# Kernel tuning notes

Hardware: AMD Instinct MI355X
Metric: run time of the kernel (lower is better)

## Reference

```python
import jax, jax.numpy as jnp
import numpy as np

TOPK = 2  # config.expert_topk


def setup_inputs() -> dict:
    key = jax.random.key(0)
    k1, k2, k3, k4 = jax.random.split(key, 4)
    B, T, D, H, E = 2, 2048, 768, 3072, 8
    x = jax.random.normal(k1, (B, T, D), jnp.float32)
    gate_w = jax.random.normal(k2, (E, D), jnp.float32) * 0.02   # nn.Linear(D, E).weight
    w_fc = jax.random.normal(k3, (E, H, D), jnp.float32) * 0.02  # per-expert c_fc.weight [out,in]
    w_proj = jax.random.normal(k4, (E, D, H), jnp.float32) * 0.02  # per-expert c_proj.weight
    return {"x": x, "gate_w": gate_w, "w_fc": w_fc, "w_proj": w_proj}


def reference(x, gate_w, w_fc, w_proj):
    # x: [B,T,D]; gate_w: [E,D]; w_fc: [E,H,D]; w_proj: [E,D,H]
    B, T, D = x.shape
    E = gate_w.shape[0]
    N = B * T
    xf = x.reshape(N, D)

    gate_logits = xf @ gate_w.T                       # [N,E]
    gate_probs = jax.nn.softmax(gate_logits, axis=-1)
    rw, idx = jax.lax.top_k(gate_probs, TOPK)          # [N,k]
    rw = rw / jnp.sum(rw, axis=-1, keepdims=True)

    # combine[n,e] = sum_k rw[n,k] * (idx[n,k]==e); zero for unselected experts,
    # so the dense per-expert MLP below computes the same math as torch dispatch.
    oh = jax.nn.one_hot(idx, E, dtype=xf.dtype)        # [N,k,E]
    combine = jnp.einsum('nk,nke->ne', rw, oh)         # [N,E]

    h = jnp.einsum('nd,ehd->neh', xf, w_fc)            # [N,E,H]
    h = jnp.square(jax.nn.relu(h))                     # relu(x)^2
    y = jnp.einsum('neh,edh->ned', h, w_proj)          # [N,E,D]
    out = jnp.einsum('ned,ne->nd', y, combine).reshape(B, T, D)

    # expert_freq = bincount(expert_indices)/N, detached in the loss
    counts = jnp.sum(oh, axis=(0, 1))                  # [E]
    expert_freq = counts / N
    balance_loss = jnp.sum(gate_probs.mean(axis=0) * jax.lax.stop_gradient(expert_freq)) * E
    return out, balance_loss
```

## Files before the change

kernel.cpp:

```cpp
#include <hip/hip_runtime.h>
#include <hip/hip_bf16.h>

typedef __bf16 bf16_t;
typedef bf16_t bf16x8 __attribute__((ext_vector_type(8)));
typedef bf16_t bf16x4 __attribute__((ext_vector_type(4)));
typedef float f32x4 __attribute__((ext_vector_type(4)));

#define N_TOK 4096
#define DIM   768
#define HID   3072
#define NEXP  8
#define PADROWS 9216
#define MMAX  32
#define MT2   64

#define OFF_COUNTS 0
#define OFF_PSUM   32
#define OFF_OFFPAD 64
#define OFF_CURSOR 128
#define OFF_TOKE   256
#define OFF_TOKW   (OFF_TOKE + 4*8192)
#define OFF_PERMT  (OFF_TOKW + 4*8192)
#define OFF_PERMW  (OFF_PERMT + 4*PADROWS)
#define OFF_XP     (((OFF_PERMW + 4*PADROWS) + 511) & ~511ull)
#define OFF_WFC    (OFF_XP + 2ull*PADROWS*DIM)
#define OFF_WPJ    (OFF_WFC + 2ull*NEXP*HID*DIM)
#define OFF_H      (OFF_WPJ + 2ull*NEXP*DIM*HID)
#define WS_NEEDED  (OFF_H + 2ull*PADROWS*HID)

#define CONV_BLOCKS 9216
#define GATE_BLOCKS (N_TOK / 4)

__device__ __forceinline__ void async_copy16(const bf16_t* g, bf16_t* l) {
    __builtin_amdgcn_global_load_lds(
        (const __attribute__((address_space(1))) void*)g,
        (__attribute__((address_space(3))) void*)l, 16, 0, 0);
}

__global__ __launch_bounds__(256) void prep_kernel(
    const float* __restrict__ w_fc, const float* __restrict__ w_proj,
    bf16_t* __restrict__ wfc_b, bf16_t* __restrict__ wpj_b,
    const float* __restrict__ x, const float* __restrict__ gw,
    int* __restrict__ cs_part, float* __restrict__ ps_part,
    int* __restrict__ tok_e, float* __restrict__ tok_w)
{
    __shared__ float ps[8];
    __shared__ int cs[8];

    if (blockIdx.x >= GATE_BLOCKS) {
        const int cid = blockIdx.x - GATE_BLOCKS;
        const int half_blocks = CONV_BLOCKS / 2;
        const bool second = cid >= half_blocks;
        const float* src = second ? w_proj : w_fc;
        bf16_t* dst = second ? wpj_b : wfc_b;
        const long long bid = second ? (cid - half_blocks) : cid;
        const long long base = bid * 256 + threadIdx.x;
        const long long stride = (long long)half_blocks * 256;
#pragma unroll
        for (int it = 0; it < 4; it++) {
            const long long i4 = base + (long long)it * stride;
            float4 v = *((const float4*)src + i4);
            bf16x4 o;
            o[0] = (bf16_t)v.x; o[1] = (bf16_t)v.y;
            o[2] = (bf16_t)v.z; o[3] = (bf16_t)v.w;
            *(bf16x4*)(dst + i4 * 4) = o;
        }
        return;
    }

    if (threadIdx.x < 8) { ps[threadIdx.x] = 0.f; cs[threadIdx.x] = 0; }
    __syncthreads();

    const int bid = blockIdx.x;
    const int wv = threadIdx.x >> 6, lane = threadIdx.x & 63;
    const int n = bid * 4 + wv;

    float acc[8];
#pragma unroll
    for (int e = 0; e < 8; e++) acc[e] = 0.f;
    const float* xr = x + (size_t)n * DIM;
#pragma unroll
    for (int c = 0; c < 12; c++) {
        const float xv = xr[c * 64 + lane];
#pragma unroll
        for (int e = 0; e < 8; e++) acc[e] += xv * gw[e * DIM + c * 64 + lane];
    }
#pragma unroll
    for (int e = 0; e < 8; e++)
        for (int off = 32; off > 0; off >>= 1) acc[e] += __shfl_xor(acc[e], off, 64);

    float mx = acc[0];
#pragma unroll
    for (int e = 1; e < 8; e++) mx = fmaxf(mx, acc[e]);
    float p[8], s = 0.f;
#pragma unroll
    for (int e = 0; e < 8; e++) { p[e] = expf(acc[e] - mx); s += p[e]; }

    int e1 = 0;
#pragma unroll
    for (int e = 1; e < 8; e++) if (p[e] > p[e1]) e1 = e;
    int e2 = (e1 == 0) ? 1 : 0;
#pragma unroll
    for (int e = 0; e < 8; e++) if (e != e1 && p[e] > p[e2]) e2 = e;
    const float denom = p[e1] + p[e2];

    if (lane == 0) {
        tok_e[2 * n] = e1; tok_e[2 * n + 1] = e2;
        tok_w[2 * n] = p[e1] / denom; tok_w[2 * n + 1] = p[e2] / denom;
        const float inv = 1.f / s;
#pragma unroll
        for (int e = 0; e < 8; e++) atomicAdd(&ps[e], p[e] * inv);
        atomicAdd(&cs[e1], 1); atomicAdd(&cs[e2], 1);
    }
    __syncthreads();
    if (threadIdx.x < 8) {
        ps_part[bid * 8 + threadIdx.x] = ps[threadIdx.x];
        cs_part[bid * 8 + threadIdx.x] = cs[threadIdx.x];
    }
}

__global__ __launch_bounds__(256) void finalize_scatter(
    const int* cs_part, const float* ps_part,
    const int* __restrict__ tok_e, const float* __restrict__ tok_w,
    int* __restrict__ counts, int* __restrict__ off_pad,
    int* perm_tok, int* inv_pos, float* __restrict__ out_loss)
{
    __shared__ float rps[256];
    __shared__ int rcs[256];
    __shared__ int s_cur[8];
    const int t = threadIdx.x;
    const int e = t & 7, chunk = t >> 3;
    float psum = 0.f; int csum = 0;
#pragma unroll
    for (int i = 0; i < 32; i++) {
        const int b = chunk * 32 + i;
        psum += ps_part[b * 8 + e];
        csum += cs_part[b * 8 + e];
    }
    rps[t] = psum; rcs[t] = csum;
    __syncthreads();
    for (int s = 128; s >= 8; s >>= 1) {
        if (t < s) { rps[t] += rps[t + s]; rcs[t] += rcs[t + s]; }
        __syncthreads();
    }
    if (t == 0) {
        int off = 0; float loss = 0.f;
        for (int k = 0; k < 8; k++) {
            counts[k] = rcs[k];
            off_pad[k] = off; s_cur[k] = off;
            off += ((rcs[k] + 127) & ~127);
            loss += rps[k] * (float)rcs[k];
        }
        off_pad[8] = off;
        *out_loss = loss * 8.f / ((float)N_TOK * (float)N_TOK);
    }
    __syncthreads();
    for (int r = 0; r < N_TOK / 256; r++) {
        const int n = r * 256 + t;
#pragma unroll
        for (int k = 0; k < 2; k++) {
            const int ee = tok_e[2 * n + k];
            const int pos = atomicAdd(&s_cur[ee], 1);
            perm_tok[pos] = n;
            inv_pos[2 * n + k] = pos;
        }
    }
}

__global__ __launch_bounds__(256) void gather_x_kernel(
    const float* __restrict__ x, const int* __restrict__ off_pad,
    const int* __restrict__ counts, const int* __restrict__ perm_tok,
    bf16_t* __restrict__ xp)
{
    __shared__ int so[9], scnt[8];
    if (threadIdx.x < 9) so[threadIdx.x] = off_pad[threadIdx.x];
    if (threadIdx.x < 8) scnt[threadIdx.x] = counts[threadIdx.x];
    __syncthreads();
    const int gid = blockIdx.x * 256 + threadIdx.x;
    const int p = gid / 192;
    const int c = (gid - p * 192) * 4;
    int e = 0;
#pragma unroll
    for (int k = 1; k < 8; k++) if (p >= so[k]) e = k;
    const bool valid = (p < so[8]) && (p - so[e] < scnt[e]);
    float4 v = make_float4(0.f, 0.f, 0.f, 0.f);
    if (valid) {
        const int tok = perm_tok[p];
        v = *(const float4*)(x + (size_t)tok * DIM + c);
    }
    bf16x4 o; o[0] = (bf16_t)v.x; o[1] = (bf16_t)v.y; o[2] = (bf16_t)v.z; o[3] = (bf16_t)v.w;
    *(bf16x4*)(xp + (size_t)p * DIM + c) = o;
}

__global__ __launch_bounds__(256, 3) void gemm1_kernel(
    const bf16_t* __restrict__ xp, const bf16_t* __restrict__ wfc,
    const int* __restrict__ off_pad, bf16_t* __restrict__ h)
{
    const int id = blockIdx.x;
    const int e = id & 7;
    const int slot = id >> 3;
    const int n_t = slot / MMAX, m_t = slot % MMAX;

    const int seg0 = off_pad[e];
    const int cnt_pad = off_pad[e + 1] - seg0;
    const int m0 = m_t * 128;
    if (m0 >= cnt_pad) return;
    const int n0 = n_t * 128;

    __shared__ bf16_t As[128 * 64];
    __shared__ bf16_t Bs[128 * 64];

    const int t = threadIdx.x;
    const int srow = t >> 3, sc = t & 7;
    const int gsc = sc ^ (srow & 7);
    const bf16_t* abase = xp + (size_t)(seg0 + m0 + srow) * DIM + gsc * 8;
    const bf16_t* bbase = wfc + ((size_t)e * HID + n0 + srow) * DIM + gsc * 8;

    const int wv = t >> 6, lane = t & 63;
    const int lrow = lane & 15, quad = lane >> 4;
    const int wm = (wv & 1) * 64, wn = (wv >> 1) * 64;
    const int sw = lrow & 7;

    f32x4 acc[4][4] = {};

    for (int k0 = 0; k0 < DIM; k0 += 64) {
        __syncthreads();
#pragma unroll
        for (int ii = 0; ii < 4; ii++) {
            async_copy16(abase + (size_t)ii * 32 * DIM + k0, &As[(ii * 256 + t) * 8]);
            async_copy16(bbase + (size_t)ii * 32 * DIM + k0, &Bs[(ii * 256 + t) * 8]);
        }
        __syncthreads();
#pragma unroll
        for (int kh = 0; kh < 2; kh++) {
            const int ch = ((kh * 4 + quad) ^ sw) * 8;
            bf16x8 af[4], bfv[4];
#pragma unroll
            for (int i = 0; i < 4; i++)
                af[i] = *(bf16x8*)&As[(wm + i * 16 + lrow) * 64 + ch];
#pragma unroll
            for (int j = 0; j < 4; j++)
                bfv[j] = *(bf16x8*)&Bs[(wn + j * 16 + lrow) * 64 + ch];
#pragma unroll
            for (int i = 0; i < 4; i++)
#pragma unroll
                for (int j = 0; j < 4; j++)
                    acc[i][j] = __builtin_amdgcn_mfma_f32_16x16x32_bf16(af[i], bfv[j], acc[i][j], 0, 0, 0);
        }
    }

#pragma unroll
    for (int i = 0; i < 4; i++) {
#pragma unroll
        for (int g = 0; g < 4; g++) {
            const int m = m0 + wm + i * 16 + quad * 4 + g;
            bf16_t* hrow = h + (size_t)(seg0 + m) * HID + n0 + wn + lrow;
#pragma unroll
            for (int j = 0; j < 4; j++) {
                float v = fmaxf(acc[i][j][g], 0.f);
                hrow[j * 16] = (bf16_t)(v * v);
            }
        }
    }
}

__global__ __launch_bounds__(256, 3) void gemm2_kernel(
    const bf16_t* __restrict__ h, const bf16_t* __restrict__ wpj,
    const int* __restrict__ off_pad, const int* __restrict__ counts,
    bf16_t* __restrict__ y)
{
    const int id = blockIdx.x;
    const int e = id & 7;
    const int slot = id >> 3;
    const int m_t = slot / 6, n_t = slot % 6;

    const int seg0 = off_pad[e];
    const int cnt = counts[e];
    const int m0 = m_t * 64;
    if (m0 >= cnt) return;
    const int n0 = n_t * 128;

    __shared__ bf16_t As[64 * 128];
    __shared__ bf16_t Bs[128 * 128];

    const int t = threadIdx.x;
    const int srow = t >> 4, sc = t & 15;
    const int gsc = sc ^ (srow & 7);
    const bf16_t* abase = h + (size_t)(seg0 + m0 + srow) * HID + gsc * 8;
    const bf16_t* bbase = wpj + ((size_t)e * DIM + n0 + srow) * HID + gsc * 8;

    const int wv = t >> 6, lane = t & 63;
    const int lrow = lane & 15, quad = lane >> 4;
    const int wm = (wv & 1) * 32, wn = (wv >> 1) * 64;
    const int sw = lrow & 7;

    f32x4 acc[2][4] = {};

    for (int k0 = 0; k0 < HID; k0 += 128) {
        __syncthreads();
#pragma unroll
        for (int ii = 0; ii < 4; ii++)
            async_copy16(abase + (size_t)ii * 16 * HID + k0, &As[(ii * 256 + t) * 8]);
#pragma unroll
        for (int ii = 0; ii < 8; ii++)
            async_copy16(bbase + (size_t)ii * 16 * HID + k0, &Bs[(ii * 256 + t) * 8]);
        __syncthreads();
#pragma unroll
        for (int kh = 0; kh < 4; kh++) {
            const int ch = ((kh * 4 + quad) ^ sw) * 8;
            bf16x8 af[2], bfv[4];
#pragma unroll
            for (int i = 0; i < 2; i++)
                af[i] = *(bf16x8*)&As[(wm + i * 16 + lrow) * 128 + ch];
#pragma unroll
            for (int j = 0; j < 4; j++)
                bfv[j] = *(bf16x8*)&Bs[(wn + j * 16 + lrow) * 128 + ch];
#pragma unroll
            for (int i = 0; i < 2; i++)
#pragma unroll
                for (int j = 0; j < 4; j++)
                    acc[i][j] = __builtin_amdgcn_mfma_f32_16x16x32_bf16(af[i], bfv[j], acc[i][j], 0, 0, 0);
        }
    }

#pragma unroll
    for (int i = 0; i < 2; i++) {
#pragma unroll
        for (int g = 0; g < 4; g++) {
            const int m = m0 + wm + i * 16 + quad * 4 + g;
            if (m < cnt) {
                bf16_t* yrow = y + (size_t)(seg0 + m) * DIM + n0 + wn + lrow;
#pragma unroll
                for (int j = 0; j < 4; j++)
                    yrow[j * 16] = (bf16_t)acc[i][j][g];
            }
        }
    }
}

__global__ __launch_bounds__(192) void combine_kernel(
    const bf16_t* __restrict__ y, const int* __restrict__ inv_pos,
    const float* __restrict__ tok_w, float* __restrict__ out)
{
    const int n = blockIdx.x;
    const int d = threadIdx.x * 4;
    const int p1 = inv_pos[2 * n], p2 = inv_pos[2 * n + 1];
    const float w1 = tok_w[2 * n], w2 = tok_w[2 * n + 1];
    bf16x4 a = *(const bf16x4*)(y + (size_t)p1 * DIM + d);
    bf16x4 b = *(const bf16x4*)(y + (size_t)p2 * DIM + d);
    float4 o;
    o.x = w1 * (float)a[0] + w2 * (float)b[0];
    o.y = w1 * (float)a[1] + w2 * (float)b[1];
    o.z = w1 * (float)a[2] + w2 * (float)b[2];
    o.w = w1 * (float)a[3] + w2 * (float)b[3];
    *(float4*)(out + (size_t)n * DIM + d) = o;
}

extern "C" void kernel_launch(void* const* d_in, const int* in_sizes, int n_in,
                              void* d_out, int out_size, void* d_ws, size_t ws_size,
                              hipStream_t stream) {
    const float* x      = (const float*)d_in[0];
    const float* gate_w = (const float*)d_in[1];
    const float* w_fc   = (const float*)d_in[2];
    const float* w_proj = (const float*)d_in[3];
    float* out = (float*)d_out;

    if (ws_size < WS_NEEDED) return;

    char* w = (char*)d_ws;
    int*    counts    = (int*)(w + OFF_COUNTS);
    int*    off_pad   = (int*)(w + OFF_OFFPAD);
    int*    tok_e     = (int*)(w + OFF_TOKE);
    float*  tok_w     = (float*)(w + OFF_TOKW);
    int*    perm_tok  = (int*)(w + OFF_PERMT);
    int*    inv_pos   = (int*)(w + OFF_PERMW);
    bf16_t* xp        = (bf16_t*)(w + OFF_XP);
    bf16_t* wfc_b     = (bf16_t*)(w + OFF_WFC);
    bf16_t* wpj_b     = (bf16_t*)(w + OFF_WPJ);
    bf16_t* hbuf      = (bf16_t*)(w + OFF_H);

    int*   cs_part = perm_tok;
    float* ps_part = (float*)inv_pos;
    bf16_t* y = xp;

    hipMemsetAsync(d_out, 0, (size_t)out_size * sizeof(float), stream);

    prep_kernel<<<GATE_BLOCKS + CONV_BLOCKS, 256, 0, stream>>>(
        w_fc, w_proj, wfc_b, wpj_b, x, gate_w, cs_part, ps_part, tok_e, tok_w);
    finalize_scatter<<<1, 256, 0, stream>>>(cs_part, ps_part, tok_e, tok_w,
                                            counts, off_pad, perm_tok, inv_pos,
                                            out + (size_t)out_size - 1);
    gather_x_kernel<<<PADROWS * DIM / 4 / 256, 256, 0, stream>>>(x, off_pad, counts, perm_tok, xp);

    gemm1_kernel<<<8 * 24 * MMAX, 256, 0, stream>>>(xp, wfc_b, off_pad, hbuf);
    gemm2_kernel<<<8 * MT2 * 6, 256, 0, stream>>>(hbuf, wpj_b, off_pad, counts, y);
    combine_kernel<<<N_TOK, 192, 0, stream>>>(y, inv_pos, tok_w, out);
}
```

Measured before the change: 337.6 us.

## Overlap w_proj conversion with gemm1 and split gemm2 LDS tiles into halves

Converting w_proj to bf16 moves out of the prep kernel and into extra trailing blocks of the gemm1 launch. The aim is to overlap that bandwidth-bound conversion with the expert GEMM and to shorten the critical prep phase. Separately, gemm2's 128-wide K tile in LDS is split into two 64-wide sub-tiles so the 8-chunk XOR swizzle covers each row fully, which reduces LDS bank conflicts. The extra conversion blocks compete with gemm1 blocks for CUs and may delay the GEMM tail.

```diff
diff --git a/kernel.cpp b/kernel.cpp
--- a/kernel.cpp
+++ b/kernel.cpp
@@ -28,8 +28,9 @@
 #define OFF_H      (OFF_WPJ + 2ull*NEXP*DIM*HID)
 #define WS_NEEDED  (OFF_H + 2ull*PADROWS*HID)
 
-#define CONV_BLOCKS 9216
 #define GATE_BLOCKS (N_TOK / 4)
+#define CONVH_BLOCKS 4608
+#define GEMM1_BLOCKS (8 * 24 * MMAX)
 
 __device__ __forceinline__ void async_copy16(const bf16_t* g, bf16_t* l) {
     __builtin_amdgcn_global_load_lds(
@@ -37,9 +38,24 @@
         (__attribute__((address_space(3))) void*)l, 16, 0, 0);
 }
 
+__device__ __forceinline__ void convert_chunk(const float* __restrict__ src,
+                                              bf16_t* __restrict__ dst,
+                                              int cid, int t) {
+    const long long base = (long long)cid * 256 + t;
+    const long long stride = (long long)CONVH_BLOCKS * 256;
+#pragma unroll
+    for (int it = 0; it < 4; it++) {
+        const long long i4 = base + (long long)it * stride;
+        float4 v = *((const float4*)src + i4);
+        bf16x4 o;
+        o[0] = (bf16_t)v.x; o[1] = (bf16_t)v.y;
+        o[2] = (bf16_t)v.z; o[3] = (bf16_t)v.w;
+        *(bf16x4*)(dst + i4 * 4) = o;
+    }
+}
+
 __global__ __launch_bounds__(256) void prep_kernel(
-    const float* __restrict__ w_fc, const float* __restrict__ w_proj,
-    bf16_t* __restrict__ wfc_b, bf16_t* __restrict__ wpj_b,
+    const float* __restrict__ w_fc, bf16_t* __restrict__ wfc_b,
     const float* __restrict__ x, const float* __restrict__ gw,
     int* __restrict__ cs_part, float* __restrict__ ps_part,
     int* __restrict__ tok_e, float* __restrict__ tok_w)
@@ -48,23 +64,7 @@
     __shared__ int cs[8];
 
     if (blockIdx.x >= GATE_BLOCKS) {
-        const int cid = blockIdx.x - GATE_BLOCKS;
-        const int half_blocks = CONV_BLOCKS / 2;
-        const bool second = cid >= half_blocks;
-        const float* src = second ? w_proj : w_fc;
-        bf16_t* dst = second ? wpj_b : wfc_b;
-        const long long bid = second ? (cid - half_blocks) : cid;
-        const long long base = bid * 256 + threadIdx.x;
-        const long long stride = (long long)half_blocks * 256;
-#pragma unroll
-        for (int it = 0; it < 4; it++) {
-            const long long i4 = base + (long long)it * stride;
-            float4 v = *((const float4*)src + i4);
-            bf16x4 o;
-            o[0] = (bf16_t)v.x; o[1] = (bf16_t)v.y;
-            o[2] = (bf16_t)v.z; o[3] = (bf16_t)v.w;
-            *(bf16x4*)(dst + i4 * 4) = o;
-        }
+        convert_chunk(w_fc, wfc_b, blockIdx.x - GATE_BLOCKS, threadIdx.x);
         return;
     }
 
@@ -194,9 +194,14 @@
 
 __global__ __launch_bounds__(256, 3) void gemm1_kernel(
     const bf16_t* __restrict__ xp, const bf16_t* __restrict__ wfc,
-    const int* __restrict__ off_pad, bf16_t* __restrict__ h)
+    const int* __restrict__ off_pad, bf16_t* __restrict__ h,
+    const float* __restrict__ w_proj, bf16_t* __restrict__ wpj_b)
 {
     const int id = blockIdx.x;
+    if (id >= GEMM1_BLOCKS) {
+        convert_chunk(w_proj, wpj_b, id - GEMM1_BLOCKS, threadIdx.x);
+        return;
+    }
     const int e = id & 7;
     const int slot = id >> 3;
     const int n_t = slot / MMAX, m_t = slot % MMAX;
@@ -280,11 +285,11 @@
     if (m0 >= cnt) return;
     const int n0 = n_t * 128;
 
-    __shared__ bf16_t As[64 * 128];
-    __shared__ bf16_t Bs[128 * 128];
+    __shared__ bf16_t As[2][64 * 64];
+    __shared__ bf16_t Bs[2][128 * 64];
 
     const int t = threadIdx.x;
-    const int srow = t >> 4, sc = t & 15;
+    const int srow = t >> 3, sc = t & 7;
     const int gsc = sc ^ (srow & 7);
     const bf16_t* abase = h + (size_t)(seg0 + m0 + srow) * HID + gsc * 8;
     const bf16_t* bbase = wpj + ((size_t)e * DIM + n0 + srow) * HID + gsc * 8;
@@ -299,22 +304,28 @@
     for (int k0 = 0; k0 < HID; k0 += 128) {
         __syncthreads();
 #pragma unroll
-        for (int ii = 0; ii < 4; ii++)
-            async_copy16(abase + (size_t)ii * 16 * HID + k0, &As[(ii * 256 + t) * 8]);
-#pragma unroll
-        for (int ii = 0; ii < 8; ii++)
-            async_copy16(bbase + (size_t)ii * 16 * HID + k0, &Bs[(ii * 256 + t) * 8]);
+        for (int p = 0; p < 2; p++) {
+#pragma unroll
+            for (int ii = 0; ii < 2; ii++)
+                async_copy16(abase + (size_t)ii * 32 * HID + k0 + p * 64,
+                             &As[p][(ii * 256 + t) * 8]);
+#pragma unroll
+            for (int ii = 0; ii < 4; ii++)
+                async_copy16(bbase + (size_t)ii * 32 * HID + k0 + p * 64,
+                             &Bs[p][(ii * 256 + t) * 8]);
+        }
         __syncthreads();
 #pragma unroll
         for (int kh = 0; kh < 4; kh++) {
-            const int ch = ((kh * 4 + quad) ^ sw) * 8;
+            const int p = kh >> 1, khh = kh & 1;
+            const int ch = ((khh * 4 + quad) ^ sw) * 8;
             bf16x8 af[2], bfv[4];
 #pragma unroll
             for (int i = 0; i < 2; i++)
-                af[i] = *(bf16x8*)&As[(wm + i * 16 + lrow) * 128 + ch];
+                af[i] = *(bf16x8*)&As[p][(wm + i * 16 + lrow) * 64 + ch];
 #pragma unroll
             for (int j = 0; j < 4; j++)
-                bfv[j] = *(bf16x8*)&Bs[(wn + j * 16 + lrow) * 128 + ch];
+                bfv[j] = *(bf16x8*)&Bs[p][(wn + j * 16 + lrow) * 64 + ch];
 #pragma unroll
             for (int i = 0; i < 2; i++)
 #pragma unroll
@@ -385,14 +396,15 @@
 
     hipMemsetAsync(d_out, 0, (size_t)out_size * sizeof(float), stream);
 
-    prep_kernel<<<GATE_BLOCKS + CONV_BLOCKS, 256, 0, stream>>>(
-        w_fc, w_proj, wfc_b, wpj_b, x, gate_w, cs_part, ps_part, tok_e, tok_w);
+    prep_kernel<<<GATE_BLOCKS + CONVH_BLOCKS, 256, 0, stream>>>(
+        w_fc, wfc_b, x, gate_w, cs_part, ps_part, tok_e, tok_w);
     finalize_scatter<<<1, 256, 0, stream>>>(cs_part, ps_part, tok_e, tok_w,
                                             counts, off_pad, perm_tok, inv_pos,
                                             out + (size_t)out_size - 1);
     gather_x_kernel<<<PADROWS * DIM / 4 / 256, 256, 0, stream>>>(x, off_pad, counts, perm_tok, xp);
 
-    gemm1_kernel<<<8 * 24 * MMAX, 256, 0, stream>>>(xp, wfc_b, off_pad, hbuf);
+    gemm1_kernel<<<GEMM1_BLOCKS + CONVH_BLOCKS, 256, 0, stream>>>(
+        xp, wfc_b, off_pad, hbuf, w_proj, wpj_b);
     gemm2_kernel<<<8 * MT2 * 6, 256, 0, stream>>>(hbuf, wpj_b, off_pad, counts, y);
     combine_kernel<<<N_TOK, 192, 0, stream>>>(y, inv_pos, tok_w, out);
 }
```

After: 323.0 us. 1.05x faster.
